# Kernel optimization log

Measured on AMD Instinct MI355X. Metric: run time of the kernel, lower is better.

Reference implementation:

```python
import jax, jax.numpy as jnp
import numpy as np

B, H, S, D = 2, 12, 1024, 128
KQ, KK = 6, 11  # per-head conv kernel over (query, key) score plane


def setup_inputs() -> dict:
    key = jax.random.key(0)
    kq, kk, kv, kw = jax.random.split(key, 4)
    Q = jax.random.normal(kq, (B, H, S, D), dtype=jnp.float32)
    K = jax.random.normal(kk, (B, H, S, D), dtype=jnp.float32)
    V = jax.random.normal(kv, (B, H, S, D), dtype=jnp.float32)
    W = jax.random.normal(kw, (H, KQ, KK), dtype=jnp.float32) * 0.1
    return {"Q": Q, "K": K, "V": V, "W": W}


def reference(Q, K, V, W):
    # causal=True, softmax_scale = 1/sqrt(head_dim)  (module defaults)
    b, h, s, d = Q.shape
    _, kq, kk = W.shape
    pad_q = kq - 1            # causal padding along the query axis
    pad_k = (kk - 1) // 2     # 'same' padding along the key axis
    scale = 1.0 / np.sqrt(d).astype(np.float32)

    # Raw QK^T scores: [b, h, s_q, s_k]
    scores = jnp.einsum('bhqd,bhkd->bhqk', Q, K)

    # Causal: zero out future keys before the conv so the kernel cannot mix
    # in future information (matches the `causal` flag passed into the
    # fused qk_conv kernel; out-of-range tiles load as 0 in the Triton code).
    tril = jnp.tril(jnp.ones((s, s), dtype=bool))
    scores = jnp.where(tril[None, None], scores, 0.0)

    # Per-head 2D conv over the (q, k) plane: grouped conv with H groups,
    # kernel W[h] applied to head h's score map. Cross-correlation (PyTorch
    # conv semantics == lax.conv_general_dilated without kernel flip).
    conv = jax.lax.conv_general_dilated(
        scores,                      # [b, h, s, s] as NCHW
        W[:, None, :, :],            # [h, 1, kq, kk] as OIHW, groups=h
        window_strides=(1, 1),
        padding=((pad_q, 0), (pad_k, pad_k)),
        feature_group_count=h,
        dimension_numbers=('NCHW', 'OIHW', 'NCHW'),
    )

    # Scale, re-apply causal mask with the kernel's -1e6 fill, softmax, @V.
    logits = conv * scale + jnp.where(tril[None, None], 0.0, -1000000.0)
    P = jax.nn.softmax(logits, axis=-1)
    O = jnp.einsum('bhqk,bhkd->bhqd', P, V)
    return O
```

## Files before the change

### kernel.cpp

```cpp
#include <hip/hip_runtime.h>
#include <hip/hip_bf16.h>
#include <math.h>

#define B_ 2
#define H_ 12
#define S_ 1024
#define D_ 128
#define TQ 32
#define TK 32
#define NW 4
#define SCALE 0.08838834764831843f

#define QROWS (S_ + 16)
#define KROWS (16 + S_ + 16)

#define QBLK 3120
#define KBLK 3168
#define VBLK 3072

typedef __attribute__((ext_vector_type(8))) short short8;
typedef __attribute__((ext_vector_type(4))) float floatx4;

__device__ __forceinline__ unsigned short f2b(float f) {
    return __builtin_bit_cast(unsigned short, __float2bfloat16(f));
}

__global__ __launch_bounds__(256) void prep_kernel(
    const float* __restrict__ Q, const float* __restrict__ K,
    const float* __restrict__ V,
    unsigned short* __restrict__ Qp, unsigned short* __restrict__ Kp,
    unsigned short* __restrict__ Vt)
{
    __shared__ float ls[32][33];
    const int bid = blockIdx.x;
    const int tid = threadIdx.x;
    if (bid < QBLK) {
        int e0 = (bid * 256 + tid) * 4;
        int bh = e0 / (QROWS * D_);
        int rem = e0 - bh * (QROWS * D_);
        int r = rem >> 7, d = rem & 127;
        int sr = r - 16;
        float4 v = make_float4(0.f, 0.f, 0.f, 0.f);
        if (sr >= 0 && sr < S_) v = *(const float4*)(Q + ((size_t)bh * S_ + sr) * D_ + d);
        ushort4 o; o.x = f2b(v.x); o.y = f2b(v.y); o.z = f2b(v.z); o.w = f2b(v.w);
        *(ushort4*)(Qp + ((size_t)bh * QROWS + r) * D_ + d) = o;
    } else if (bid < QBLK + KBLK) {
        int e0 = ((bid - QBLK) * 256 + tid) * 4;
        int bh = e0 / (KROWS * D_);
        int rem = e0 - bh * (KROWS * D_);
        int r = rem >> 7, d = rem & 127;
        int sr = r - 16;
        float4 v = make_float4(0.f, 0.f, 0.f, 0.f);
        if (sr >= 0 && sr < S_) v = *(const float4*)(K + ((size_t)bh * S_ + sr) * D_ + d);
        ushort4 o; o.x = f2b(v.x); o.y = f2b(v.y); o.z = f2b(v.z); o.w = f2b(v.w);
        *(ushort4*)(Kp + ((size_t)bh * KROWS + r) * D_ + d) = o;
    } else {
        int b = bid - (QBLK + KBLK);
        int dt = b & 3; int kt = (b >> 2) & 31; int bh = b >> 7;
        int lk = tid >> 3, ld = (tid & 7) * 4;
        float4 v = *(const float4*)(V + ((size_t)bh * S_ + kt * 32 + lk) * D_ + dt * 32 + ld);
        ls[lk][ld + 0] = v.x; ls[lk][ld + 1] = v.y; ls[lk][ld + 2] = v.z; ls[lk][ld + 3] = v.w;
        __syncthreads();
        int lk2 = tid >> 3, lc = (tid & 7) * 4;
        ushort4 o;
        o.x = f2b(ls[lc + 0][lk2]); o.y = f2b(ls[lc + 1][lk2]);
        o.z = f2b(ls[lc + 2][lk2]); o.w = f2b(ls[lc + 3][lk2]);
        *(ushort4*)(Vt + ((size_t)bh * D_ + dt * 32 + lk2) * S_ + kt * 32 + lc) = o;
    }
}

__global__ __launch_bounds__(256, 2) void conv_attn_mfma(
    const unsigned short* __restrict__ Qp,
    const unsigned short* __restrict__ Kp,
    const unsigned short* __restrict__ Vt,
    const float* __restrict__ W,
    float* __restrict__ O)
{
    __shared__ __align__(16) unsigned short Qs[48][136];
    __shared__ __align__(16) union {
        float sc[NW][48][52];
        float oacc[32][132];
    } u;
    __shared__ float m_all[NW][32], l_all[NW][32], ms_s[32], inv_s[32];

    const int tid = threadIdx.x;
    const int wv = tid >> 6;
    const int ln = tid & 63;
    const int l15 = ln & 15;
    const int qd = ln >> 4;

    const int bid = blockIdx.x;
    const int bh = bid % (B_ * H_);
    const int qt = (S_ / TQ - 1) - bid / (B_ * H_);
    const int h = bh % H_;
    const int q0 = qt * TQ;

    const unsigned short* Qb = Qp + (size_t)bh * QROWS * D_;
    const unsigned short* Kb = Kp + (size_t)bh * KROWS * D_;
    const unsigned short* Vb = Vt + (size_t)bh * D_ * S_;
    const float* Wh = W + h * 66;

    for (int idx = tid; idx < 48 * 16; idx += 256) {
        int r = idx >> 4, c8 = (idx & 15) * 8;
        *(short8*)&Qs[r][c8] = *(const short8*)(Qb + (size_t)(q0 + r) * D_ + c8);
    }
    __syncthreads();

    floatx4 acc[2][8];
    #pragma unroll
    for (int mt = 0; mt < 2; ++mt)
        #pragma unroll
        for (int nt = 0; nt < 8; ++nt)
            acc[mt][nt] = (floatx4){0.f, 0.f, 0.f, 0.f};
    float m_run[2] = {-INFINITY, -INFINITY};
    float l_run[2] = {0.f, 0.f};

    const int nkt = qt + 1;
    for (int kt = wv; kt < nkt; kt += NW) {
        const int k0 = kt * TK;

        #pragma unroll
        for (int nt = 0; nt < 3; ++nt) {
            const unsigned short* krow = Kb + (size_t)(k0 + 8 + nt * 16 + l15) * D_;
            short8 kf[4];
            #pragma unroll
            for (int kc = 0; kc < 4; ++kc)
                kf[kc] = *(const short8*)(krow + kc * 32 + qd * 8);
            #pragma unroll
            for (int mt = 0; mt < 3; ++mt) {
                floatx4 s = {0.f, 0.f, 0.f, 0.f};
                #pragma unroll
                for (int kc = 0; kc < 4; ++kc) {
                    short8 qf = *(const short8*)&Qs[mt * 16 + l15][kc * 32 + qd * 8];
                    s = __builtin_amdgcn_mfma_f32_16x16x32_bf16(qf, kf[kc], s, 0, 0, 0);
                }
                const int qrow = q0 - 16 + mt * 16 + qd * 4;
                const int kcol = k0 - 8 + nt * 16 + l15;
                #pragma unroll
                for (int reg = 0; reg < 4; ++reg)
                    u.sc[wv][mt * 16 + qd * 4 + reg][nt * 16 + l15] =
                        (kcol <= qrow + reg) ? s[reg] : 0.f;
            }
        }

        short8 vf[8];
        #pragma unroll
        for (int nt = 0; nt < 8; ++nt)
            vf[nt] = *(const short8*)(Vb + (size_t)(nt * 16 + l15) * S_ + k0 + qd * 8);

        float pl[2][8];
        #pragma unroll
        for (int mt2 = 0; mt2 < 2; ++mt2)
            #pragma unroll
            for (int jj = 0; jj < 8; ++jj) pl[mt2][jj] = 0.f;
        #pragma unroll
        for (int mt2 = 0; mt2 < 2; ++mt2) {
            #pragma unroll
            for (int i = 0; i < 6; ++i) {
                const float* rp = &u.sc[wv][l15 + 11 + 16 * mt2 + i][qd * 8];
                float4 a0 = ((const float4*)rp)[0];
                float4 a1 = ((const float4*)rp)[1];
                float4 a2 = ((const float4*)rp)[2];
                float4 a3 = ((const float4*)rp)[3];
                float4 a4 = ((const float4*)rp)[4];
                float2 a5 = *(const float2*)(rp + 20);
                float win[22] = {a0.x, a0.y, a0.z, a0.w, a1.x, a1.y, a1.z, a1.w,
                                 a2.x, a2.y, a2.z, a2.w, a3.x, a3.y, a3.z, a3.w,
                                 a4.x, a4.y, a4.z, a4.w, a5.x, a5.y};
                #pragma unroll
                for (int j = 0; j < 11; ++j) {
                    const float w = Wh[i * 11 + j];
                    #pragma unroll
                    for (int jj = 0; jj < 8; ++jj)
                        pl[mt2][jj] = fmaf(w, win[3 + j + jj], pl[mt2][jj]);
                }
            }
        }

        float al[2];
        short8 pfrag[2];
        #pragma unroll
        for (int mt2 = 0; mt2 < 2; ++mt2) {
            const int qrow = q0 + l15 + 16 * mt2;
            float lg[8];
            float mx = -1e30f;
            #pragma unroll
            for (int jj = 0; jj < 8; ++jj) {
                const int kcol = k0 + qd * 8 + jj;
                lg[jj] = (kcol <= qrow) ? pl[mt2][jj] * SCALE : -1e30f;
                mx = fmaxf(mx, lg[jj]);
            }
            mx = fmaxf(mx, __shfl_xor(mx, 16));
            mx = fmaxf(mx, __shfl_xor(mx, 32));
            const float nm = fmaxf(m_run[mt2], mx);
            al[mt2] = __expf(m_run[mt2] - nm);
            float sum = 0.f;
            short8 pb;
            #pragma unroll
            for (int jj = 0; jj < 8; ++jj) {
                float p = __expf(lg[jj] - nm);
                sum += p;
                pb[jj] = (short)f2b(p);
            }
            sum += __shfl_xor(sum, 16);
            sum += __shfl_xor(sum, 32);
            l_run[mt2] = l_run[mt2] * al[mt2] + sum;
            m_run[mt2] = nm;
            pfrag[mt2] = pb;
        }

        #pragma unroll
        for (int mt = 0; mt < 2; ++mt) {
            #pragma unroll
            for (int reg = 0; reg < 4; ++reg) {
                const float af = __shfl(al[mt], qd * 4 + reg, 64);
                #pragma unroll
                for (int nt = 0; nt < 8; ++nt)
                    acc[mt][nt][reg] *= af;
            }
        }

        #pragma unroll
        for (int nt = 0; nt < 8; ++nt)
            #pragma unroll
            for (int mt = 0; mt < 2; ++mt)
                acc[mt][nt] = __builtin_amdgcn_mfma_f32_16x16x32_bf16(pfrag[mt], vf[nt], acc[mt][nt], 0, 0, 0);
    }

    if (qd == 0) {
        m_all[wv][l15] = m_run[0]; m_all[wv][l15 + 16] = m_run[1];
        l_all[wv][l15] = l_run[0]; l_all[wv][l15 + 16] = l_run[1];
    }
    __syncthreads();
    if (tid < 32) {
        float ms = -INFINITY;
        #pragma unroll
        for (int w = 0; w < NW; ++w) ms = fmaxf(ms, m_all[w][tid]);
        float ls = 0.f;
        #pragma unroll
        for (int w = 0; w < NW; ++w) ls += __expf(m_all[w][tid] - ms) * l_all[w][tid];
        ms_s[tid] = ms;
        inv_s[tid] = 1.f / ls;
    }
    __syncthreads();
    for (int w = 0; w < NW; ++w) {
        if (wv == w) {
            #pragma unroll
            for (int mt = 0; mt < 2; ++mt) {
                #pragma unroll
                for (int reg = 0; reg < 4; ++reg) {
                    const int row = mt * 16 + qd * 4 + reg;
                    const float f = __expf(m_all[wv][row] - ms_s[row]);
                    #pragma unroll
                    for (int nt = 0; nt < 8; ++nt) {
                        const float val = acc[mt][nt][reg] * f;
                        if (w == 0) u.oacc[row][nt * 16 + l15] = val;
                        else        u.oacc[row][nt * 16 + l15] += val;
                    }
                }
            }
        }
        __syncthreads();
    }

    {
        const int r = tid >> 3;
        const int c0 = (tid & 7) * 16;
        const float inv = inv_s[r];
        float* orow = O + ((size_t)bh * S_ + q0 + r) * D_ + c0;
        #pragma unroll
        for (int g = 0; g < 4; ++g) {
            float4 o;
            o.x = u.oacc[r][c0 + g * 4 + 0] * inv;
            o.y = u.oacc[r][c0 + g * 4 + 1] * inv;
            o.z = u.oacc[r][c0 + g * 4 + 2] * inv;
            o.w = u.oacc[r][c0 + g * 4 + 3] * inv;
            *(float4*)(orow + g * 4) = o;
        }
    }
}

extern "C" void kernel_launch(void* const* d_in, const int* in_sizes, int n_in,
                              void* d_out, int out_size, void* d_ws, size_t ws_size,
                              hipStream_t stream) {
    const float* Q = (const float*)d_in[0];
    const float* K = (const float*)d_in[1];
    const float* V = (const float*)d_in[2];
    const float* W = (const float*)d_in[3];
    float* O = (float*)d_out;

    unsigned short* Qp = (unsigned short*)d_ws;
    unsigned short* Kp = (unsigned short*)((char*)d_ws + 6389760);
    unsigned short* Vt = (unsigned short*)((char*)d_ws + 12877824);

    prep_kernel<<<dim3(QBLK + KBLK + VBLK), dim3(256), 0, stream>>>(Q, K, V, Qp, Kp, Vt);
    conv_attn_mfma<<<dim3(B_ * H_ * (S_ / TQ)), dim3(256), 0, stream>>>(Qp, Kp, Vt, W, O);
}
```

Before: 240.3 us.

## Use 64-row query tiles with all waves cooperating on each key tile

Query tiles double to 64 rows. All four waves now work together on each 32-key tile instead of splitting key tiles across waves: they share the QK^T halo tiles, the conv/softmax rows and the P@V output columns, exchanging data through shared memory. This cuts the redundant halo score work per output and removes the end-of-kernel merge of per-wave softmax and accumulator state. The block-to-head mapping is also reordered. The cost is two block barriers per key tile, half as many blocks to fill the GPU, and serial per-block work that grows with causal length.

```diff
diff --git a/kernel.cpp b/kernel.cpp
--- a/kernel.cpp
+++ b/kernel.cpp
@@ -6,9 +6,8 @@
 #define H_ 12
 #define S_ 1024
 #define D_ 128
-#define TQ 32
+#define TQ 64
 #define TK 32
-#define NW 4
 #define SCALE 0.08838834764831843f
 
 #define QROWS (S_ + 16)
@@ -76,12 +75,10 @@
     const float* __restrict__ W,
     float* __restrict__ O)
 {
-    __shared__ __align__(16) unsigned short Qs[48][136];
-    __shared__ __align__(16) union {
-        float sc[NW][48][52];
-        float oacc[32][132];
-    } u;
-    __shared__ float m_all[NW][32], l_all[NW][32], ms_s[32], inv_s[32];
+    __shared__ __align__(16) unsigned short Qs[80][136];
+    __shared__ __align__(16) float sc[80][52];
+    __shared__ __align__(16) unsigned short P[2][64][40];
+    __shared__ __align__(16) float al_s[2][64];
 
     const int tid = threadIdx.x;
     const int wv = tid >> 6;
@@ -90,8 +87,8 @@
     const int qd = ln >> 4;
 
     const int bid = blockIdx.x;
-    const int bh = bid % (B_ * H_);
-    const int qt = (S_ / TQ - 1) - bid / (B_ * H_);
+    const int bh = (bid & 7) * 3 + ((bid >> 3) % 3);
+    const int qt = 15 - bid / 24;
     const int h = bh % H_;
     const int q0 = qt * TQ;
 
@@ -100,182 +97,171 @@
     const unsigned short* Vb = Vt + (size_t)bh * D_ * S_;
     const float* Wh = W + h * 66;
 
-    for (int idx = tid; idx < 48 * 16; idx += 256) {
+    for (int idx = tid; idx < 80 * 16; idx += 256) {
         int r = idx >> 4, c8 = (idx & 15) * 8;
         *(short8*)&Qs[r][c8] = *(const short8*)(Qb + (size_t)(q0 + r) * D_ + c8);
     }
     __syncthreads();
 
-    floatx4 acc[2][8];
+    int nt_t[4], mt_t[4], kro_t[4];
     #pragma unroll
-    for (int mt = 0; mt < 2; ++mt)
-        #pragma unroll
-        for (int nt = 0; nt < 8; ++nt)
-            acc[mt][nt] = (floatx4){0.f, 0.f, 0.f, 0.f};
-    float m_run[2] = {-INFINITY, -INFINITY};
-    float l_run[2] = {0.f, 0.f};
-
-    const int nkt = qt + 1;
-    for (int kt = wv; kt < nkt; kt += NW) {
+    for (int t = 0; t < 4; ++t) {
+        int u = wv * 4 + t;
+        int nt = u / 5;
+        nt_t[t] = nt; mt_t[t] = u - nt * 5;
+        kro_t[t] = 8 + nt * 16 + l15;
+    }
+
+    const int p = 16 * wv + (ln >> 2);
+    const int c0 = (ln & 3) * 8;
+
+    floatx4 acc[4][2];
+    #pragma unroll
+    for (int mt = 0; mt < 4; ++mt)
+        #pragma unroll
+        for (int n2 = 0; n2 < 2; ++n2)
+            acc[mt][n2] = (floatx4){0.f, 0.f, 0.f, 0.f};
+    float m_run = -INFINITY, l_run = 0.f;
+
+    const int nkt = 2 * qt + 2;
+    for (int kt = 0; kt < nkt; ++kt) {
         const int k0 = kt * TK;
-
-        #pragma unroll
-        for (int nt = 0; nt < 3; ++nt) {
-            const unsigned short* krow = Kb + (size_t)(k0 + 8 + nt * 16 + l15) * D_;
-            short8 kf[4];
-            #pragma unroll
-            for (int kc = 0; kc < 4; ++kc)
-                kf[kc] = *(const short8*)(krow + kc * 32 + qd * 8);
-            #pragma unroll
-            for (int mt = 0; mt < 3; ++mt) {
+        const int par = kt & 1;
+
+        #pragma unroll
+        for (int t = 0; t < 4; ++t) {
+            if (wv * 4 + t < 15) {
+                const int nt = nt_t[t], mt = mt_t[t];
+                const unsigned short* krow = Kb + (size_t)(k0 + kro_t[t]) * D_;
+                short8 kf[4], qf[4];
+                #pragma unroll
+                for (int kc = 0; kc < 4; ++kc) {
+                    kf[kc] = *(const short8*)(krow + kc * 32 + qd * 8);
+                    qf[kc] = *(const short8*)&Qs[mt * 16 + l15][kc * 32 + qd * 8];
+                }
                 floatx4 s = {0.f, 0.f, 0.f, 0.f};
                 #pragma unroll
-                for (int kc = 0; kc < 4; ++kc) {
-                    short8 qf = *(const short8*)&Qs[mt * 16 + l15][kc * 32 + qd * 8];
-                    s = __builtin_amdgcn_mfma_f32_16x16x32_bf16(qf, kf[kc], s, 0, 0, 0);
-                }
+                for (int kc = 0; kc < 4; ++kc)
+                    s = __builtin_amdgcn_mfma_f32_16x16x32_bf16(qf[kc], kf[kc], s, 0, 0, 0);
                 const int qrow = q0 - 16 + mt * 16 + qd * 4;
                 const int kcol = k0 - 8 + nt * 16 + l15;
                 #pragma unroll
                 for (int reg = 0; reg < 4; ++reg)
-                    u.sc[wv][mt * 16 + qd * 4 + reg][nt * 16 + l15] =
+                    sc[mt * 16 + qd * 4 + reg][nt * 16 + l15] =
                         (kcol <= qrow + reg) ? s[reg] : 0.f;
             }
         }
-
-        short8 vf[8];
-        #pragma unroll
-        for (int nt = 0; nt < 8; ++nt)
-            vf[nt] = *(const short8*)(Vb + (size_t)(nt * 16 + l15) * S_ + k0 + qd * 8);
-
-        float pl[2][8];
-        #pragma unroll
-        for (int mt2 = 0; mt2 < 2; ++mt2)
-            #pragma unroll
-            for (int jj = 0; jj < 8; ++jj) pl[mt2][jj] = 0.f;
-        #pragma unroll
-        for (int mt2 = 0; mt2 < 2; ++mt2) {
-            #pragma unroll
-            for (int i = 0; i < 6; ++i) {
-                const float* rp = &u.sc[wv][l15 + 11 + 16 * mt2 + i][qd * 8];
-                float4 a0 = ((const float4*)rp)[0];
-                float4 a1 = ((const float4*)rp)[1];
-                float4 a2 = ((const float4*)rp)[2];
-                float4 a3 = ((const float4*)rp)[3];
-                float4 a4 = ((const float4*)rp)[4];
-                float2 a5 = *(const float2*)(rp + 20);
-                float win[22] = {a0.x, a0.y, a0.z, a0.w, a1.x, a1.y, a1.z, a1.w,
-                                 a2.x, a2.y, a2.z, a2.w, a3.x, a3.y, a3.z, a3.w,
-                                 a4.x, a4.y, a4.z, a4.w, a5.x, a5.y};
-                #pragma unroll
-                for (int j = 0; j < 11; ++j) {
-                    const float w = Wh[i * 11 + j];
-                    #pragma unroll
-                    for (int jj = 0; jj < 8; ++jj)
-                        pl[mt2][jj] = fmaf(w, win[3 + j + jj], pl[mt2][jj]);
-                }
-            }
-        }
-
-        float al[2];
-        short8 pfrag[2];
-        #pragma unroll
-        for (int mt2 = 0; mt2 < 2; ++mt2) {
-            const int qrow = q0 + l15 + 16 * mt2;
+        __syncthreads();
+
+        float pl[8];
+        #pragma unroll
+        for (int jj = 0; jj < 8; ++jj) pl[jj] = 0.f;
+        #pragma unroll
+        for (int i = 0; i < 6; ++i) {
+            const float* rp = &sc[p + 11 + i][c0];
+            float4 b0 = ((const float4*)rp)[0];
+            float4 b1 = ((const float4*)rp)[1];
+            float4 b2 = ((const float4*)rp)[2];
+            float4 b3 = ((const float4*)rp)[3];
+            float4 b4 = ((const float4*)rp)[4];
+            float4 b5 = ((const float4*)rp)[5];
+            float win[24] = {b0.x, b0.y, b0.z, b0.w, b1.x, b1.y, b1.z, b1.w,
+                             b2.x, b2.y, b2.z, b2.w, b3.x, b3.y, b3.z, b3.w,
+                             b4.x, b4.y, b4.z, b4.w, b5.x, b5.y, b5.z, b5.w};
+            #pragma unroll
+            for (int j = 0; j < 11; ++j) {
+                const float w = Wh[i * 11 + j];
+                #pragma unroll
+                for (int jj = 0; jj < 8; ++jj)
+                    pl[jj] = fmaf(w, win[3 + j + jj], pl[jj]);
+            }
+        }
+
+        {
+            const int q = q0 + p;
             float lg[8];
             float mx = -1e30f;
             #pragma unroll
             for (int jj = 0; jj < 8; ++jj) {
-                const int kcol = k0 + qd * 8 + jj;
-                lg[jj] = (kcol <= qrow) ? pl[mt2][jj] * SCALE : -1e30f;
+                const int k = k0 + c0 + jj;
+                lg[jj] = (k <= q) ? pl[jj] * SCALE : -1e30f;
                 mx = fmaxf(mx, lg[jj]);
             }
-            mx = fmaxf(mx, __shfl_xor(mx, 16));
-            mx = fmaxf(mx, __shfl_xor(mx, 32));
-            const float nm = fmaxf(m_run[mt2], mx);
-            al[mt2] = __expf(m_run[mt2] - nm);
+            mx = fmaxf(mx, __shfl_xor(mx, 1));
+            mx = fmaxf(mx, __shfl_xor(mx, 2));
+            const float nm = fmaxf(m_run, mx);
+            const float alpha = __expf(m_run - nm);
             float sum = 0.f;
             short8 pb;
             #pragma unroll
             for (int jj = 0; jj < 8; ++jj) {
-                float p = __expf(lg[jj] - nm);
-                sum += p;
-                pb[jj] = (short)f2b(p);
-            }
-            sum += __shfl_xor(sum, 16);
-            sum += __shfl_xor(sum, 32);
-            l_run[mt2] = l_run[mt2] * al[mt2] + sum;
-            m_run[mt2] = nm;
-            pfrag[mt2] = pb;
-        }
-
-        #pragma unroll
-        for (int mt = 0; mt < 2; ++mt) {
+                float pv = __expf(lg[jj] - nm);
+                sum += pv;
+                pb[jj] = (short)f2b(pv);
+            }
+            sum += __shfl_xor(sum, 1);
+            sum += __shfl_xor(sum, 2);
+            l_run = l_run * alpha + sum;
+            m_run = nm;
+            *(short8*)&P[par][p][c0] = pb;
+            if ((ln & 3) == 0) al_s[par][p] = alpha;
+        }
+        __syncthreads();
+
+        {
+            float4 al4[4];
+            #pragma unroll
+            for (int mt = 0; mt < 4; ++mt)
+                al4[mt] = *(const float4*)&al_s[par][mt * 16 + qd * 4];
+            #pragma unroll
+            for (int mt = 0; mt < 4; ++mt) {
+                #pragma unroll
+                for (int n2 = 0; n2 < 2; ++n2) {
+                    acc[mt][n2][0] *= al4[mt].x;
+                    acc[mt][n2][1] *= al4[mt].y;
+                    acc[mt][n2][2] *= al4[mt].z;
+                    acc[mt][n2][3] *= al4[mt].w;
+                }
+            }
+            short8 pf[4];
+            #pragma unroll
+            for (int mt = 0; mt < 4; ++mt)
+                pf[mt] = *(const short8*)&P[par][mt * 16 + l15][qd * 8];
+            short8 vfr[2];
+            #pragma unroll
+            for (int n2 = 0; n2 < 2; ++n2) {
+                const int d = (2 * wv + n2) * 16 + l15;
+                vfr[n2] = *(const short8*)(Vb + (size_t)d * S_ + k0 + qd * 8);
+            }
+            #pragma unroll
+            for (int n2 = 0; n2 < 2; ++n2)
+                #pragma unroll
+                for (int mt = 0; mt < 4; ++mt)
+                    acc[mt][n2] = __builtin_amdgcn_mfma_f32_16x16x32_bf16(pf[mt], vfr[n2], acc[mt][n2], 0, 0, 0);
+        }
+    }
+
+    __syncthreads();
+    if ((ln & 3) == 0) al_s[0][p] = 1.0f / l_run;
+    __syncthreads();
+    {
+        float4 inv4[4];
+        #pragma unroll
+        for (int mt = 0; mt < 4; ++mt)
+            inv4[mt] = *(const float4*)&al_s[0][mt * 16 + qd * 4];
+        float* Ob = O + (size_t)bh * S_ * D_;
+        #pragma unroll
+        for (int mt = 0; mt < 4; ++mt) {
+            const float iv[4] = {inv4[mt].x, inv4[mt].y, inv4[mt].z, inv4[mt].w};
             #pragma unroll
             for (int reg = 0; reg < 4; ++reg) {
-                const float af = __shfl(al[mt], qd * 4 + reg, 64);
-                #pragma unroll
-                for (int nt = 0; nt < 8; ++nt)
-                    acc[mt][nt][reg] *= af;
-            }
-        }
-
-        #pragma unroll
-        for (int nt = 0; nt < 8; ++nt)
-            #pragma unroll
-            for (int mt = 0; mt < 2; ++mt)
-                acc[mt][nt] = __builtin_amdgcn_mfma_f32_16x16x32_bf16(pfrag[mt], vf[nt], acc[mt][nt], 0, 0, 0);
-    }
-
-    if (qd == 0) {
-        m_all[wv][l15] = m_run[0]; m_all[wv][l15 + 16] = m_run[1];
-        l_all[wv][l15] = l_run[0]; l_all[wv][l15 + 16] = l_run[1];
-    }
-    __syncthreads();
-    if (tid < 32) {
-        float ms = -INFINITY;
-        #pragma unroll
-        for (int w = 0; w < NW; ++w) ms = fmaxf(ms, m_all[w][tid]);
-        float ls = 0.f;
-        #pragma unroll
-        for (int w = 0; w < NW; ++w) ls += __expf(m_all[w][tid] - ms) * l_all[w][tid];
-        ms_s[tid] = ms;
-        inv_s[tid] = 1.f / ls;
-    }
-    __syncthreads();
-    for (int w = 0; w < NW; ++w) {
-        if (wv == w) {
-            #pragma unroll
-            for (int mt = 0; mt < 2; ++mt) {
-                #pragma unroll
-                for (int reg = 0; reg < 4; ++reg) {
-                    const int row = mt * 16 + qd * 4 + reg;
-                    const float f = __expf(m_all[wv][row] - ms_s[row]);
-                    #pragma unroll
-                    for (int nt = 0; nt < 8; ++nt) {
-                        const float val = acc[mt][nt][reg] * f;
-                        if (w == 0) u.oacc[row][nt * 16 + l15] = val;
-                        else        u.oacc[row][nt * 16 + l15] += val;
-                    }
+                const int row = mt * 16 + qd * 4 + reg;
+                #pragma unroll
+                for (int n2 = 0; n2 < 2; ++n2) {
+                    const int col = (2 * wv + n2) * 16 + l15;
+                    Ob[(size_t)(q0 + row) * D_ + col] = acc[mt][n2][reg] * iv[reg];
                 }
             }
-        }
-        __syncthreads();
-    }
-
-    {
-        const int r = tid >> 3;
-        const int c0 = (tid & 7) * 16;
-        const float inv = inv_s[r];
-        float* orow = O + ((size_t)bh * S_ + q0 + r) * D_ + c0;
-        #pragma unroll
-        for (int g = 0; g < 4; ++g) {
-            float4 o;
-            o.x = u.oacc[r][c0 + g * 4 + 0] * inv;
-            o.y = u.oacc[r][c0 + g * 4 + 1] * inv;
-            o.z = u.oacc[r][c0 + g * 4 + 2] * inv;
-            o.w = u.oacc[r][c0 + g * 4 + 3] * inv;
-            *(float4*)(orow + g * 4) = o;
         }
     }
 }
```

Result: faster. 233.6 us (-2.8%).
